# Kernel optimization log

Measured on AMD Instinct MI355X. Metric: run time of the kernel, lower is better.

The kernel has to match this reference:

```python
import jax, jax.numpy as jnp
import numpy as np

DIM = 512
HEADS = 8
DIM_HEAD = 64
VID = (8, 32, 32)   # (frames, height, width)
KS = (3, 3, 3)      # odd kernel sizes
DIL = (1, 1, 1)


def _build_indices():
    F, H, W = VID
    kf, kh, kw = KS
    df, dh, dw = DIL
    pf, ph, pw = df * (kf - 1) // 2, dh * (kh - 1) // 2, dw * (kw - 1) // 2
    Fp, Hp, Wp = F + 2 * pf, H + 2 * ph, W + 2 * pw
    N = F * H * W
    ff, yy, xx = np.meshgrid(np.arange(F), np.arange(H), np.arange(W), indexing='ij')
    of, oy, ox = np.meshgrid(np.arange(kf) * df, np.arange(kh) * dh, np.arange(kw) * dw, indexing='ij')
    nf = ff[..., None, None, None] + of   # (F,H,W,kf,kh,kw) coords in padded volume
    ny = yy[..., None, None, None] + oy
    nx = xx[..., None, None, None] + ox
    nbr = ((nf * Hp + ny) * Wp + nx).reshape(N, -1)  # (N, K) flat indices into padded volume
    sf, sy, sx = nf - pf, ny - ph, nx - pw           # source coords in unpadded volume
    valid = (sf >= 0) & (sf < F) & (sy >= 0) & (sy < H) & (sx >= 0) & (sx < W)
    tok = np.where(valid, (sf * H + sy) * W + sx, N).reshape(N, -1)  # sentinel N = padding
    mask = np.arange(N)[:, None] < tok               # causal mask; sentinel N always masked
    mask = np.concatenate([np.zeros((N, 1), bool), mask], axis=1)    # bos column never masked
    return jnp.asarray(nbr), jnp.asarray(mask), ((pf, pf), (ph, ph), (pw, pw))

_NBR, _MASK, _PAD = _build_indices()


def setup_inputs() -> dict:
    key = jax.random.key(0)
    ks = jax.random.split(key, 6)
    F, H, W = VID
    n = F * H * W + 1
    inner = HEADS * DIM_HEAD
    s = DIM ** -0.5
    return {
        "x":     jax.random.normal(ks[0], (1, n, DIM), jnp.float32),
        "w_q":   jax.random.normal(ks[1], (DIM, inner), jnp.float32) * s,
        "w_kv":  jax.random.normal(ks[2], (DIM, 2 * inner), jnp.float32) * s,
        "w_th":  jax.random.normal(ks[3], (HEADS, HEADS), jnp.float32) * HEADS ** -0.5,
        "w_out": jax.random.normal(ks[4], (inner, DIM), jnp.float32) * inner ** -0.5,
        "b_out": jnp.zeros((DIM,), jnp.float32),
    }


def reference(x, w_q, w_kv, w_th, w_out, b_out):
    b, n, _ = x.shape
    F, H, W = VID
    N = F * H * W  # n == N + 1 (BOS token first)
    h, d = HEADS, DIM_HEAD
    q = x @ w_q
    k, v = jnp.split(x @ w_kv, 2, axis=-1)

    def heads(t):
        return t.reshape(b, n, h, d).transpose(0, 2, 1, 3).reshape(b * h, n, d)

    q = heads(q) * d ** -0.5
    k, v = heads(k), heads(v)
    q = q[:, 1:]
    k_bos, k = k[:, :1], k[:, 1:]
    v_bos, v = v[:, :1], v[:, 1:]

    def unfold(t):  # gather 3D local neighborhoods: (bh, N, d) -> (bh, N, K, d)
        vol = jnp.pad(t.reshape(b * h, F, H, W, d), ((0, 0),) + _PAD + ((0, 0),))
        return vol.reshape(b * h, -1, d)[:, _NBR]

    kj = jnp.concatenate([jnp.broadcast_to(k_bos[:, None], (b * h, N, 1, d)), unfold(k)], axis=2)
    vj = jnp.concatenate([jnp.broadcast_to(v_bos[:, None], (b * h, N, 1, d)), unfold(v)], axis=2)

    sim = jnp.einsum('bid,bijd->bij', q, kj)                  # (bh, N, K+1)
    sim = jnp.where(_MASK[None], jnp.finfo(sim.dtype).min, sim)
    attn = jax.nn.softmax(sim, axis=-1)                       # stable_softmax == shift-invariant softmax
    attn = jnp.einsum('gh,bhij->bgij', w_th, attn.reshape(b, h, N, -1)).reshape(b * h, N, -1)
    out = jnp.einsum('bij,bijd->bid', attn, vj)               # (bh, N, d)
    out = jnp.concatenate([v_bos, out], axis=1)               # prepend bos value passthrough
    out = out.reshape(b, h, n, d).transpose(0, 2, 1, 3).reshape(b, n, h * d)
    return out @ w_out + b_out
```

## Files before the change

kernel.cpp:

```cpp
#include <hip/hip_runtime.h>
#include <stdint.h>

#define DIMC 512
#define INNER 512
#define NTOK 8192
#define NSEQ 8193
#define MPAD 8320
#define QKV_COLS 1536

#define CONV_XT   (MPAD * DIMC / 4)
#define CONV_WQKV (QKV_COLS * DIMC)
#define CONV_WOUT (INNER * DIMC)
#define CONV_TOT  (CONV_XT + CONV_WQKV + CONV_WOUT)

typedef __attribute__((ext_vector_type(8))) short bf16x8;
typedef __attribute__((ext_vector_type(4))) float f32x4;
typedef __attribute__((ext_vector_type(8))) unsigned short u16x8;

__device__ __forceinline__ float bf2f(unsigned short u) {
  return __uint_as_float(((unsigned int)u) << 16);
}
__device__ __forceinline__ unsigned short f2bf(float f) {
  unsigned int x = __float_as_uint(f);
  unsigned int lsb = (x >> 16) & 1u;
  x += 0x7fffu + lsb;
  return (unsigned short)(x >> 16);
}

__device__ __forceinline__ void gload_lds16(const unsigned short* g, unsigned short* l) {
  __builtin_amdgcn_global_load_lds(
      (const __attribute__((address_space(1))) void*)g,
      (__attribute__((address_space(3))) void*)l, 16, 0, 0);
}

__global__ void k_conv(const float* __restrict__ x, const float* __restrict__ wq,
                       const float* __restrict__ wkv, const float* __restrict__ wout,
                       unsigned short* __restrict__ xb, unsigned short* __restrict__ wqkvT,
                       unsigned short* __restrict__ woutT) {
  const int gid = blockIdx.x * 256 + threadIdx.x;
  if (gid < CONV_XT) {
    const int idx = gid * 4;
    const int row = idx / DIMC;
    ushort4 o;
    if (row < NSEQ) {
      const float4 v = *(const float4*)(x + idx);
      o.x = f2bf(v.x); o.y = f2bf(v.y); o.z = f2bf(v.z); o.w = f2bf(v.w);
    } else {
      o.x = 0; o.y = 0; o.z = 0; o.w = 0;
    }
    *(ushort4*)(xb + idx) = o;
  } else if (gid < CONV_XT + CONV_WQKV) {
    const int idx = gid - CONV_XT;
    const int c = idx / DIMC, k = idx % DIMC;
    const float v = (c < INNER) ? wq[k * INNER + c] * 0.125f
                                : wkv[k * (2 * INNER) + (c - INNER)];
    wqkvT[idx] = f2bf(v);
  } else {
    const int idx = gid - CONV_XT - CONV_WQKV;
    const int c = idx / DIMC, k = idx % DIMC;
    woutT[idx] = f2bf(wout[k * DIMC + c]);
  }
}

template <int BN, int TN, int LDC, bool OUT_BF16>
__global__ __launch_bounds__(256)
void k_gemm(const unsigned short* __restrict__ A,
            const unsigned short* __restrict__ BT,
            void* __restrict__ C,
            const float* __restrict__ bias,
            int Mreal) {
  __shared__ unsigned short As[128 * 64];
  __shared__ unsigned short Bs[BN * 64];
  constexpr int MF = (BN == 128) ? 4 : 2;
  constexpr int ISS_B = BN / 32;

  int flat;
  {
    const int nwg = (int)gridDim.x;
    const int q = nwg >> 3, r = nwg & 7;
    const int xcd = (int)blockIdx.x & 7, idx = (int)blockIdx.x >> 3;
    flat = (xcd < r ? xcd * (q + 1) : r * (q + 1) + (xcd - r) * q) + idx;
  }
  const int tm = flat / TN;
  const int tn = flat % TN;

  const int tid = (int)threadIdx.x;
  const int wave = tid >> 6;
  const int lane = tid & 63;
  const int wm = (BN == 128) ? ((wave >> 1) * 64) : (wave * 32);
  const int wn = (BN == 128) ? ((wave & 1) * 64) : 0;

  f32x4 acc[MF][4];
#pragma unroll
  for (int m = 0; m < MF; ++m)
#pragma unroll
    for (int n = 0; n < 4; ++n) {
      acc[m][n][0] = 0.f; acc[m][n][1] = 0.f; acc[m][n][2] = 0.f; acc[m][n][3] = 0.f;
    }

  const size_t a_base = (size_t)tm * 128 * DIMC;
  const size_t b_base = (size_t)tn * BN * DIMC;
  const int lrow = lane >> 3;
  const int lk = (lane & 7) * 8;

  for (int k0 = 0; k0 < DIMC; k0 += 64) {
    __syncthreads();
#pragma unroll
    for (int c = 0; c < 4; ++c) {
      const int rA = wave * 32 + c * 8;
      gload_lds16(A + a_base + (size_t)(rA + lrow) * DIMC + k0 + lk, &As[rA * 64]);
    }
#pragma unroll
    for (int c = 0; c < ISS_B; ++c) {
      const int rB = wave * (BN / 4) + c * 8;
      gload_lds16(BT + b_base + (size_t)(rB + lrow) * DIMC + k0 + lk, &Bs[rB * 64]);
    }
    __syncthreads();

    const int fr = lane & 15;
    const int kg = (lane >> 4) * 8;
#pragma unroll
    for (int kk = 0; kk < 2; ++kk) {
      bf16x8 af[MF], bfr[4];
#pragma unroll
      for (int m = 0; m < MF; ++m)
        af[m] = *(const bf16x8*)&As[(wm + m * 16 + fr) * 64 + kk * 32 + kg];
#pragma unroll
      for (int n = 0; n < 4; ++n)
        bfr[n] = *(const bf16x8*)&Bs[(wn + n * 16 + fr) * 64 + kk * 32 + kg];
#pragma unroll
      for (int m = 0; m < MF; ++m)
#pragma unroll
        for (int n = 0; n < 4; ++n)
          acc[m][n] = __builtin_amdgcn_mfma_f32_16x16x32_bf16(af[m], bfr[n], acc[m][n], 0, 0, 0);
    }
  }

  const int fr = lane & 15;
  const int rg = (lane >> 4) * 4;
#pragma unroll
  for (int m = 0; m < MF; ++m) {
#pragma unroll
    for (int r = 0; r < 4; ++r) {
      const int row = tm * 128 + wm + m * 16 + rg + r;
      if (row < Mreal) {
#pragma unroll
        for (int n = 0; n < 4; ++n) {
          const int col = tn * BN + wn + n * 16 + fr;
          const float v = acc[m][n][r];
          if constexpr (OUT_BF16) {
            ((unsigned short*)C)[(size_t)row * LDC + col] = f2bf(v);
          } else {
            ((float*)C)[(size_t)row * LDC + col] = v + bias[col];
          }
        }
      }
    }
  }
}

__global__ __launch_bounds__(256)
void k_attn3(const unsigned short* __restrict__ qkv, const float* __restrict__ w_th,
             unsigned short* __restrict__ Ob) {
  const int bid = (int)blockIdx.x;
  const int t = (int)threadIdx.x;
  if (bid == NTOK / 4) {
    *(unsigned int*)(Ob + 2 * t) = *(const unsigned int*)(qkv + 2 * INNER + 2 * t);
    return;
  }
  const int blk = ((bid & 7) << 8) | (bid >> 3);
  const int w = t >> 6;
  const int l = t & 63;
  const int i = blk * 4 + w;
  const int e = l & 7;
  const int gbase = l & 56;

  int my_pack = -1;
  {
    const int f = i >> 10, rr = i & 1023, y = rr >> 5, xx = rr & 31;
    const int a = l / 9, rem = l % 9, bb = rem / 3, cc = rem % 3;
    const int sf = f + a - 1, sy = y + bb - 1, sx = xx + cc - 1;
    if (l < 27 && (unsigned)sf < 8u && (unsigned)sy < 32u && (unsigned)sx < 32u) {
      const int tk = (sf << 10) | (sy << 5) | sx;
      if (tk <= i) my_pack = tk + 1;
    }
  }
  const unsigned long long mask0 = __ballot(my_pack >= 0);
  const int nval = __popcll(mask0);

  float qf[8];
  {
    const u16x8 q8 = *(const u16x8*)(qkv + (size_t)(i + 1) * QKV_COLS + l * 8);
#pragma unroll
    for (int u = 0; u < 8; ++u) qf[u] = bf2f(q8[u]);
  }

  float s[4] = {-1e30f, -1e30f, -1e30f, -1e30f};
  const unsigned short* kbase = qkv + INNER + l * 8;
  {
    const u16x8 k8 = *(const u16x8*)kbase;
    float p = 0.f;
#pragma unroll
    for (int u = 0; u < 8; ++u) p = fmaf(qf[u], bf2f(k8[u]), p);
    p += __shfl_xor(p, 1); p += __shfl_xor(p, 2); p += __shfl_xor(p, 4);
    if (e == 0) s[0] = p;
  }
  {
    unsigned long long mask = mask0;
    for (int it = 0; it < nval; it += 2) {
      const int l0 = (int)__builtin_ctzll(mask);
      mask &= mask - 1;
      const bool has1 = (it + 1) < nval;
      const int l1 = mask ? (int)__builtin_ctzll(mask) : 0;
      mask &= mask - 1;
      const int pk0 = __shfl(my_pack, l0);
      const int pk1r = __shfl(my_pack, l1);
      const int pk1 = has1 ? pk1r : 0;
      const u16x8 ka = *(const u16x8*)(kbase + (size_t)pk0 * QKV_COLS);
      const u16x8 kb = *(const u16x8*)(kbase + (size_t)pk1 * QKV_COLS);
      float p0 = 0.f, p1 = 0.f;
#pragma unroll
      for (int u = 0; u < 8; ++u) {
        p0 = fmaf(qf[u], bf2f(ka[u]), p0);
        p1 = fmaf(qf[u], bf2f(kb[u]), p1);
      }
      p0 += __shfl_xor(p0, 1); p1 += __shfl_xor(p1, 1);
      p0 += __shfl_xor(p0, 2); p1 += __shfl_xor(p1, 2);
      p0 += __shfl_xor(p0, 4); p1 += __shfl_xor(p1, 4);
      {
        const int js = l0 + 1;
        const bool mine = (e == (js & 7));
        const int pp = js >> 3;
        s[0] = (mine && pp == 0) ? p0 : s[0];
        s[1] = (mine && pp == 1) ? p0 : s[1];
        s[2] = (mine && pp == 2) ? p0 : s[2];
        s[3] = (mine && pp == 3) ? p0 : s[3];
      }
      {
        const int js = l1 + 1;
        const bool mine = has1 && (e == (js & 7));
        const int pp = js >> 3;
        s[0] = (mine && pp == 0) ? p1 : s[0];
        s[1] = (mine && pp == 1) ? p1 : s[1];
        s[2] = (mine && pp == 2) ? p1 : s[2];
        s[3] = (mine && pp == 3) ? p1 : s[3];
      }
    }
  }

  float mx = fmaxf(fmaxf(s[0], s[1]), fmaxf(s[2], s[3]));
  mx = fmaxf(mx, __shfl_xor(mx, 1));
  mx = fmaxf(mx, __shfl_xor(mx, 2));
  mx = fmaxf(mx, __shfl_xor(mx, 4));
  float a4[4]; float sum = 0.f;
#pragma unroll
  for (int p = 0; p < 4; ++p) { a4[p] = __expf(s[p] - mx); sum += a4[p]; }
  sum += __shfl_xor(sum, 1); sum += __shfl_xor(sum, 2); sum += __shfl_xor(sum, 4);
  const float inv = 1.0f / sum;
#pragma unroll
  for (int p = 0; p < 4; ++p) a4[p] *= inv;

  float wth[8];
  {
    const float4 w0 = *(const float4*)(w_th + gbase);
    const float4 w1 = *(const float4*)(w_th + gbase + 4);
    wth[0] = w0.x; wth[1] = w0.y; wth[2] = w0.z; wth[3] = w0.w;
    wth[4] = w1.x; wth[5] = w1.y; wth[6] = w1.z; wth[7] = w1.w;
  }
  float m4[4];
#pragma unroll
  for (int p = 0; p < 4; ++p) {
    float acc = 0.f;
#pragma unroll
    for (int h2 = 0; h2 < 8; ++h2)
      acc = fmaf(wth[h2], __shfl(a4[p], (h2 << 3) | e), acc);
    m4[p] = acc;
  }

  float acc8[8] = {0.f, 0.f, 0.f, 0.f, 0.f, 0.f, 0.f, 0.f};
  float accb[8] = {0.f, 0.f, 0.f, 0.f, 0.f, 0.f, 0.f, 0.f};
  const unsigned short* vbase = qkv + 2 * INNER + l * 8;
  {
    const float mv = __shfl(m4[0], gbase);
    const u16x8 v8 = *(const u16x8*)vbase;
#pragma unroll
    for (int u = 0; u < 8; ++u) acc8[u] = fmaf(mv, bf2f(v8[u]), acc8[u]);
  }
  {
    unsigned long long mask = mask0;
    for (int it = 0; it < nval; it += 2) {
      const int l0 = (int)__builtin_ctzll(mask);
      mask &= mask - 1;
      const bool has1 = (it + 1) < nval;
      const int l1 = mask ? (int)__builtin_ctzll(mask) : 0;
      mask &= mask - 1;
      const int pk0 = __shfl(my_pack, l0);
      const int pk1r = __shfl(my_pack, l1);
      const int pk1 = has1 ? pk1r : 0;
      const u16x8 va = *(const u16x8*)(vbase + (size_t)pk0 * QKV_COLS);
      const u16x8 vb = *(const u16x8*)(vbase + (size_t)pk1 * QKV_COLS);
      const int js0 = l0 + 1;
      const int pp0 = js0 >> 3;
      const float ms0 = pp0 == 0 ? m4[0] : pp0 == 1 ? m4[1] : pp0 == 2 ? m4[2] : m4[3];
      const float mv0 = __shfl(ms0, gbase | (js0 & 7));
      const int js1 = l1 + 1;
      const int pp1 = js1 >> 3;
      const float ms1 = pp1 == 0 ? m4[0] : pp1 == 1 ? m4[1] : pp1 == 2 ? m4[2] : m4[3];
      const float mv1r = __shfl(ms1, gbase | (js1 & 7));
      const float mv1 = has1 ? mv1r : 0.f;
#pragma unroll
      for (int u = 0; u < 8; ++u) {
        acc8[u] = fmaf(mv0, bf2f(va[u]), acc8[u]);
        accb[u] = fmaf(mv1, bf2f(vb[u]), accb[u]);
      }
    }
  }

  u16x8 o;
#pragma unroll
  for (int u = 0; u < 8; ++u) o[u] = f2bf(acc8[u] + accb[u]);
  *(u16x8*)(Ob + (size_t)(i + 1) * INNER + l * 8) = o;
}

extern "C" void kernel_launch(void* const* d_in, const int* in_sizes, int n_in,
                              void* d_out, int out_size, void* d_ws, size_t ws_size,
                              hipStream_t stream) {
  (void)in_sizes; (void)n_in; (void)out_size; (void)ws_size;
  const float* x     = (const float*)d_in[0];
  const float* w_q   = (const float*)d_in[1];
  const float* w_kv  = (const float*)d_in[2];
  const float* w_th  = (const float*)d_in[3];
  const float* w_out = (const float*)d_in[4];
  const float* b_out = (const float*)d_in[5];
  float* out = (float*)d_out;

  char* ws = (char*)d_ws;
  unsigned short* xb    = (unsigned short*)ws;
  unsigned short* wqkvT = (unsigned short*)(ws + 8519680);
  unsigned short* woutT = (unsigned short*)(ws + 8519680 + 1572864);
  unsigned short* qkvb  = (unsigned short*)(ws + 8519680 + 1572864 + 524288);

  k_conv<<<CONV_TOT / 256, 256, 0, stream>>>(x, w_q, w_kv, w_out, xb, wqkvT, woutT);
  k_gemm<128, QKV_COLS / 128, QKV_COLS, true>
      <<<(MPAD / 128) * (QKV_COLS / 128), 256, 0, stream>>>(xb, wqkvT, qkvb, nullptr, NSEQ);
  k_attn3<<<NTOK / 4 + 1, 256, 0, stream>>>(qkvb, w_th, xb);
  k_gemm<64, DIMC / 64, DIMC, false>
      <<<(MPAD / 128) * (DIMC / 64), 256, 0, stream>>>(xb, woutT, out, b_out, NSEQ);
}
```

Before: 75.89 us.

## Use 256x128 tiles for QKV GEMM and 2x2 spatial token blocking in attention

The QKV projection GEMM now uses 256-row tiles with 8 waves per 512-thread block, which halves the grid and raises reuse of the weight tile per block. The padded row count grows to a multiple of 256, and the workspace offsets shift to match. The attention kernel maps each 4-wave block to a 2x2 spatial patch of tokens instead of 4 consecutive x positions, so neighbouring queries share more of their 3x3x3 K/V neighbourhoods in cache. The risks are fewer, heavier blocks, which can hurt occupancy and load balance.

```diff
diff --git a/kernel.cpp b/kernel.cpp
--- a/kernel.cpp
+++ b/kernel.cpp
@@ -5,10 +5,10 @@
 #define INNER 512
 #define NTOK 8192
 #define NSEQ 8193
-#define MPAD 8320
+#define MPAD1 8448
 #define QKV_COLS 1536
 
-#define CONV_XT   (MPAD * DIMC / 4)
+#define CONV_XT   (MPAD1 * DIMC / 4)
 #define CONV_WQKV (QKV_COLS * DIMC)
 #define CONV_WOUT (INNER * DIMC)
 #define CONV_TOT  (CONV_XT + CONV_WQKV + CONV_WOUT)
@@ -62,17 +62,19 @@
   }
 }
 
-template <int BN, int TN, int LDC, bool OUT_BF16>
-__global__ __launch_bounds__(256)
+template <int BM, int BN, int TN, int LDC, bool OUT_BF16>
+__global__ __launch_bounds__((BM == 256) ? 512 : 256)
 void k_gemm(const unsigned short* __restrict__ A,
             const unsigned short* __restrict__ BT,
             void* __restrict__ C,
             const float* __restrict__ bias,
             int Mreal) {
-  __shared__ unsigned short As[128 * 64];
+  constexpr int NW = (BM == 256) ? 8 : 4;
+  constexpr int MF = (BM == 256) ? 4 : 2;
+  constexpr int ISS_A = BM / NW / 8;
+  constexpr int ISS_B = BN / NW / 8;
+  __shared__ unsigned short As[BM * 64];
   __shared__ unsigned short Bs[BN * 64];
-  constexpr int MF = (BN == 128) ? 4 : 2;
-  constexpr int ISS_B = BN / 32;
 
   int flat;
   {
@@ -87,8 +89,9 @@
   const int tid = (int)threadIdx.x;
   const int wave = tid >> 6;
   const int lane = tid & 63;
-  const int wm = (BN == 128) ? ((wave >> 1) * 64) : (wave * 32);
-  const int wn = (BN == 128) ? ((wave & 1) * 64) : 0;
+  int wm, wn;
+  if constexpr (BM == 256) { wm = (wave >> 1) * 64; wn = (wave & 1) * 64; }
+  else                     { wm = wave * 32;        wn = 0; }
 
   f32x4 acc[MF][4];
 #pragma unroll
@@ -98,7 +101,7 @@
       acc[m][n][0] = 0.f; acc[m][n][1] = 0.f; acc[m][n][2] = 0.f; acc[m][n][3] = 0.f;
     }
 
-  const size_t a_base = (size_t)tm * 128 * DIMC;
+  const size_t a_base = (size_t)tm * BM * DIMC;
   const size_t b_base = (size_t)tn * BN * DIMC;
   const int lrow = lane >> 3;
   const int lk = (lane & 7) * 8;
@@ -106,13 +109,13 @@
   for (int k0 = 0; k0 < DIMC; k0 += 64) {
     __syncthreads();
 #pragma unroll
-    for (int c = 0; c < 4; ++c) {
-      const int rA = wave * 32 + c * 8;
+    for (int c = 0; c < ISS_A; ++c) {
+      const int rA = wave * (BM / NW) + c * 8;
       gload_lds16(A + a_base + (size_t)(rA + lrow) * DIMC + k0 + lk, &As[rA * 64]);
     }
 #pragma unroll
     for (int c = 0; c < ISS_B; ++c) {
-      const int rB = wave * (BN / 4) + c * 8;
+      const int rB = wave * (BN / NW) + c * 8;
       gload_lds16(BT + b_base + (size_t)(rB + lrow) * DIMC + k0 + lk, &Bs[rB * 64]);
     }
     __syncthreads();
@@ -142,7 +145,7 @@
   for (int m = 0; m < MF; ++m) {
 #pragma unroll
     for (int r = 0; r < 4; ++r) {
-      const int row = tm * 128 + wm + m * 16 + rg + r;
+      const int row = tm * BM + wm + m * 16 + rg + r;
       if (row < Mreal) {
 #pragma unroll
         for (int n = 0; n < 4; ++n) {
@@ -171,7 +174,8 @@
   const int blk = ((bid & 7) << 8) | (bid >> 3);
   const int w = t >> 6;
   const int l = t & 63;
-  const int i = blk * 4 + w;
+  const int i = (blk >> 8 << 10) | ((((blk >> 4) & 15) * 2 + (w >> 1)) << 5)
+              | ((blk & 15) * 2 + (w & 1));
   const int e = l & 7;
   const int gbase = l & 56;
 
@@ -336,14 +340,14 @@
 
   char* ws = (char*)d_ws;
   unsigned short* xb    = (unsigned short*)ws;
-  unsigned short* wqkvT = (unsigned short*)(ws + 8519680);
-  unsigned short* woutT = (unsigned short*)(ws + 8519680 + 1572864);
-  unsigned short* qkvb  = (unsigned short*)(ws + 8519680 + 1572864 + 524288);
+  unsigned short* wqkvT = (unsigned short*)(ws + 8650752);
+  unsigned short* woutT = (unsigned short*)(ws + 10223616);
+  unsigned short* qkvb  = (unsigned short*)(ws + 10747904);
 
   k_conv<<<CONV_TOT / 256, 256, 0, stream>>>(x, w_q, w_kv, w_out, xb, wqkvT, woutT);
-  k_gemm<128, QKV_COLS / 128, QKV_COLS, true>
-      <<<(MPAD / 128) * (QKV_COLS / 128), 256, 0, stream>>>(xb, wqkvT, qkvb, nullptr, NSEQ);
+  k_gemm<256, 128, QKV_COLS / 128, QKV_COLS, true>
+      <<<(MPAD1 / 256) * (QKV_COLS / 128), 512, 0, stream>>>(xb, wqkvT, qkvb, nullptr, NSEQ);
   k_attn3<<<NTOK / 4 + 1, 256, 0, stream>>>(qkvb, w_th, xb);
-  k_gemm<64, DIMC / 64, DIMC, false>
-      <<<(MPAD / 128) * (DIMC / 64), 256, 0, stream>>>(xb, woutT, out, b_out, NSEQ);
-}
+  k_gemm<128, 64, DIMC / 64, DIMC, false>
+      <<<(8320 / 128) * (DIMC / 64), 256, 0, stream>>>(xb, woutT, out, b_out, NSEQ);
+}
```

Result: faster. 70.45 us (median of 2 runs) (-7.2%).
